# Performance work log

Hardware: AMD Instinct MI355X
Metric: run time of the kernel (lower is better)

The kernel has to match this reference:

```python
import jax, jax.numpy as jnp
import numpy as np

BATCH = 8192
IN_F = 4096
OUT_F = 4096


def setup_inputs() -> dict:
    key = jax.random.key(0)
    k_x, k_w, k_m = jax.random.split(key, 3)
    x = jax.random.normal(k_x, (BATCH, IN_F), dtype=jnp.float32)
    # kaiming_normal_ for relu: std = sqrt(2 / fan_in) with fan_in = in_features
    std = float(np.sqrt(2.0 / IN_F))
    weight = jax.random.normal(k_w, (OUT_F, IN_F), dtype=jnp.float32) * std
    bias = jnp.zeros((OUT_F,), dtype=jnp.float32)
    mask = jax.random.bernoulli(k_m, 0.5, (OUT_F, IN_F)).astype(jnp.float32)
    return {"x": x, "weight": weight, "bias": bias, "mask": mask}


def reference(x, weight, bias, mask):
    # masked_weight = weight * mask; out = x @ masked_weight.T + bias
    masked_weight = weight * mask                      # [out, in]
    return jnp.einsum("bi,oi->bo", x, masked_weight) + bias  # [batch, out]
```

## Files before the change

### kernel.cpp

```cpp
#include <hip/hip_runtime.h>
#include <stdint.h>

#define BATCH 8192
#define IN_F  4096
#define OUT_F 4096

#define BM 256
#define BN 256
#define BK 32
#define KT2 (IN_F / BK)
#define ABYTES (BM * BK * 2)
#define BUFB   (2 * ABYTES)

typedef __attribute__((ext_vector_type(8))) short bf16x8;
typedef __attribute__((ext_vector_type(4))) float f32x4;


__device__ __forceinline__ unsigned short f2bf(float f) {
    unsigned int u = __float_as_uint(f);
    unsigned int lsb = (u >> 16) & 1u;
    u += 0x7fffu + lsb;
    return (unsigned short)(u >> 16);
}

__device__ __forceinline__ void gl_lds16(const void* g, void* l) {
    __builtin_amdgcn_global_load_lds(
        (const __attribute__((address_space(1))) void*)g,
        (__attribute__((address_space(3))) void*)l,
        16, 0, 0);
}

#define XF4 (BATCH * IN_F / 4)
#define WF4 (OUT_F * IN_F / 4)

__global__ __launch_bounds__(256) void cvt_kernel(const float4* __restrict__ x,
                                                  const float4* __restrict__ w,
                                                  const float4* __restrict__ m,
                                                  uint2* __restrict__ xo,
                                                  uint2* __restrict__ wo) {
    const int i = blockIdx.x * 256 + threadIdx.x;
    union { unsigned short u[4]; uint2 v; } r;
    if (i < XF4) {
        const float4 a = x[i];
        r.u[0] = f2bf(a.x); r.u[1] = f2bf(a.y);
        r.u[2] = f2bf(a.z); r.u[3] = f2bf(a.w);
        xo[i] = r.v;
    } else {
        const int j = i - XF4;
        const float4 a = w[j];
        const float4 b = m[j];
        r.u[0] = f2bf(a.x * b.x); r.u[1] = f2bf(a.y * b.y);
        r.u[2] = f2bf(a.z * b.z); r.u[3] = f2bf(a.w * b.w);
        wo[j] = r.v;
    }
}

__global__ __launch_bounds__(512, 2) void gemm_kernel(const unsigned short* __restrict__ A,
                                                      const unsigned short* __restrict__ W,
                                                      const float* __restrict__ bias,
                                                      float* __restrict__ C) {
    __shared__ unsigned short lds[3 * BUFB / 2];

    const int tid  = threadIdx.x;
    const int lane = tid & 63;
    const int wave = tid >> 6;
    const int wm   = wave >> 2;
    const int wn   = wave & 3;

    const int wg = ((blockIdx.x & 7) << 6) | (blockIdx.x >> 3);
    const int bm = wg >> 4;
    const int bn = wg & 15;

    const int r15 = lane & 15;
    const int g   = lane >> 4;
    const int cs  = (g ^ (r15 & 3)) << 4;

    int aoff[8], boff[4];
#pragma unroll
    for (int mf = 0; mf < 8; ++mf)
        aoff[mf] = ((wm * 128 + mf * 16 + r15) << 6) + cs;
#pragma unroll
    for (int nf = 0; nf < 4; ++nf)
        boff[nf] = ABYTES + ((wn * 64 + nf * 16 + r15) << 6) + cs;

    int ldsb[4];
    const unsigned short* gA[2];
    const unsigned short* gB[2];
#pragma unroll
    for (int i = 0; i < 4; ++i) {
        const int s    = (i & 1) * 512 + tid;
        const int row  = s >> 2;
        const int chnk = (s & 3) ^ (row & 3);
        ldsb[i] = (i < 2 ? 0 : ABYTES) + s * 16;
        if (i < 2) gA[i]     = A + (size_t)(bm * BM + row) * IN_F + chnk * 8;
        else       gB[i - 2] = W + (size_t)(bn * BN + row) * IN_F + chnk * 8;
    }

    char* ldsc = (char*)lds;

#define STAGE(bufoff, ktn)                                                   \
    do {                                                                     \
        gl_lds16(gA[0] + (ktn) * BK, ldsc + (bufoff) + ldsb[0]);             \
        gl_lds16(gA[1] + (ktn) * BK, ldsc + (bufoff) + ldsb[1]);             \
        gl_lds16(gB[0] + (ktn) * BK, ldsc + (bufoff) + ldsb[2]);             \
        gl_lds16(gB[1] + (ktn) * BK, ldsc + (bufoff) + ldsb[3]);             \
    } while (0)

#define READ(AX, BX, bufoff)                                                 \
    do {                                                                     \
        _Pragma("unroll")                                                    \
        for (int mf = 0; mf < 8; ++mf)                                       \
            AX[mf] = *(const bf16x8*)(ldsc + (bufoff) + aoff[mf]);           \
        _Pragma("unroll")                                                    \
        for (int nf = 0; nf < 4; ++nf)                                       \
            BX[nf] = *(const bf16x8*)(ldsc + (bufoff) + boff[nf]);           \
    } while (0)

#define MFMA_ALL(AX, BX)                                                     \
    do {                                                                     \
        __builtin_amdgcn_s_setprio(1);                                       \
        _Pragma("unroll")                                                    \
        for (int mf = 0; mf < 8; ++mf)                                       \
            _Pragma("unroll")                                                \
            for (int nf = 0; nf < 4; ++nf)                                   \
                acc[mf][nf] = __builtin_amdgcn_mfma_f32_16x16x32_bf16(       \
                    AX[mf], BX[nf], acc[mf][nf], 0, 0, 0);                   \
        __builtin_amdgcn_s_setprio(0);                                       \
    } while (0)

#define WINDOW(kt, AC, BC, AN, BN_)                                          \
    do {                                                                     \
        if ((kt) + 1 < KT2) READ(AN, BN_, rb);                               \
        if ((kt) + 3 < KT2) STAGE(sb, (kt) + 3);                             \
        MFMA_ALL(AC, BC);                                                    \
        if ((kt) + 1 < KT2) {                                                \
            asm volatile("s_waitcnt lgkmcnt(0)" ::: "memory");               \
            __builtin_amdgcn_sched_barrier(0);                               \
            if ((kt) + 3 < KT2) { asm volatile("s_waitcnt vmcnt(4)" ::: "memory"); } \
            else                { asm volatile("s_waitcnt vmcnt(0)" ::: "memory"); } \
            __builtin_amdgcn_s_barrier();                                    \
            __builtin_amdgcn_sched_barrier(0);                               \
            int t_ = sb; sb = rb; rb = lb; lb = t_;                          \
        }                                                                    \
    } while (0)

    f32x4 acc[8][4] = {};
    bf16x8 aC[8], bC[4], aN[8], bN[4];

    STAGE(0 * BUFB, 0);
    STAGE(1 * BUFB, 1);
    STAGE(2 * BUFB, 2);
    asm volatile("s_waitcnt vmcnt(8)" ::: "memory");
    __builtin_amdgcn_s_barrier();
    __builtin_amdgcn_sched_barrier(0);

    READ(aC, bC, 0 * BUFB);
    asm volatile("s_waitcnt lgkmcnt(0)" ::: "memory");
    __builtin_amdgcn_sched_barrier(0);
    asm volatile("s_waitcnt vmcnt(4)" ::: "memory");
    __builtin_amdgcn_s_barrier();
    __builtin_amdgcn_sched_barrier(0);

    int sb = 0 * BUFB, rb = 1 * BUFB, lb = 2 * BUFB;

#pragma unroll 1
    for (int kt = 0; kt < KT2; kt += 2) {
        WINDOW(kt,     aC, bC, aN, bN);
        WINDOW(kt + 1, aN, bN, aC, bC);
    }
#undef WINDOW
#undef MFMA_ALL
#undef READ
#undef STAGE

    const int crow0 = bm * BM + wm * 128 + g * 4;
    const int ccol0 = bn * BN + wn * 64 + r15;
#pragma unroll
    for (int nf = 0; nf < 4; ++nf) {
        const int col = ccol0 + nf * 16;
        const float bj = bias[col];
#pragma unroll
        for (int mf = 0; mf < 8; ++mf)
#pragma unroll
            for (int reg = 0; reg < 4; ++reg) {
                const int row = crow0 + mf * 16 + reg;
                C[(size_t)row * OUT_F + col] = acc[mf][nf][reg] + bj;
            }
    }
}

__global__ __launch_bounds__(256) void fallback_kernel(const float* __restrict__ x,
                                                       const float* __restrict__ w,
                                                       const float* __restrict__ bias,
                                                       const float* __restrict__ m,
                                                       float* __restrict__ out) {
    size_t idx = (size_t)blockIdx.x * 256 + threadIdx.x;
    int row = (int)(idx >> 12);
    int col = (int)(idx & (OUT_F - 1));
    const float4* xr = (const float4*)(x + (size_t)row * IN_F);
    const float4* wr = (const float4*)(w + (size_t)col * IN_F);
    const float4* mr = (const float4*)(m + (size_t)col * IN_F);
    float s = 0.f;
    for (int k = 0; k < IN_F / 4; ++k) {
        float4 xv = xr[k], wv = wr[k], mv = mr[k];
        s += xv.x * wv.x * mv.x + xv.y * wv.y * mv.y +
             xv.z * wv.z * mv.z + xv.w * wv.w * mv.w;
    }
    out[idx] = s + bias[col];
}


extern "C" void kernel_launch(void* const* d_in, const int* in_sizes, int n_in,
                              void* d_out, int out_size, void* d_ws, size_t ws_size,
                              hipStream_t stream) {
    const float* x    = (const float*)d_in[0];
    const float* w    = (const float*)d_in[1];
    const float* bias = (const float*)d_in[2];
    const float* mask = (const float*)d_in[3];
    float* out = (float*)d_out;

    const size_t need = ((size_t)BATCH * IN_F + (size_t)OUT_F * IN_F) * sizeof(unsigned short);
    if (ws_size < need) {
        fallback_kernel<<<(size_t)BATCH * OUT_F / 256, 256, 0, stream>>>(
            x, w, bias, mask, out);
        return;
    }

    unsigned short* xb = (unsigned short*)d_ws;
    unsigned short* wb = xb + (size_t)BATCH * IN_F;

    cvt_kernel<<<(XF4 + WF4) / 256, 256, 0, stream>>>(
        (const float4*)x, (const float4*)w, (const float4*)mask,
        (uint2*)xb, (uint2*)wb);

    gemm_kernel<<<512, 512, 0, stream>>>(xb, wb, bias, out);
}
```

Before: 557.5 us.

## Switch GEMM to BK=64 double-buffered LDS with four-phase interleaved schedule

Doubles the K tile to 64 and replaces the triple-buffered BK=32 pipeline with two 64KB buffers. Each K step is split into four phases. Each phase reads a slice of A fragments from LDS, issues part of the next tile's global-to-LDS loads, and runs a group of MFMAs, separated by barriers. The goal is fewer loop iterations and barriers per FLOP, a smaller live fragment register set, and a finer mix of memory and MFMA work. The cost is 128KB of LDS per block and more barriers per iteration, which could stall waves if the phases are not balanced.

Result: faster. 541.2 us (-2.9%).

```diff
diff --git a/kernel.cpp b/kernel.cpp
--- a/kernel.cpp
+++ b/kernel.cpp
@@ -7,10 +7,8 @@
 
 #define BM 256
 #define BN 256
-#define BK 32
-#define KT2 (IN_F / BK)
-#define ABYTES (BM * BK * 2)
-#define BUFB   (2 * ABYTES)
+#define BK 64
+#define KT (IN_F / BK)
 
 typedef __attribute__((ext_vector_type(8))) short bf16x8;
 typedef __attribute__((ext_vector_type(4))) float f32x4;
@@ -59,7 +57,9 @@
                                                       const unsigned short* __restrict__ W,
                                                       const float* __restrict__ bias,
                                                       float* __restrict__ C) {
-    __shared__ unsigned short lds[3 * BUFB / 2];
+    __shared__ __align__(16) char smem[131072];
+    char* sA = smem;
+    char* sB = smem + 65536;
 
     const int tid  = threadIdx.x;
     const int lane = tid & 63;
@@ -73,105 +73,115 @@
 
     const int r15 = lane & 15;
     const int g   = lane >> 4;
-    const int cs  = (g ^ (r15 & 3)) << 4;
-
-    int aoff[8], boff[4];
-#pragma unroll
-    for (int mf = 0; mf < 8; ++mf)
-        aoff[mf] = ((wm * 128 + mf * 16 + r15) << 6) + cs;
-#pragma unroll
-    for (int nf = 0; nf < 4; ++nf)
-        boff[nf] = ABYTES + ((wn * 64 + nf * 16 + r15) << 6) + cs;
-
-    int ldsb[4];
-    const unsigned short* gA[2];
-    const unsigned short* gB[2];
+    const int k0  = (g ^ (r15 & 7)) << 4;
+
+    int ldso[4];
+    const unsigned short* gAp[4];
+    const unsigned short* gBp[4];
 #pragma unroll
     for (int i = 0; i < 4; ++i) {
-        const int s    = (i & 1) * 512 + tid;
-        const int row  = s >> 2;
-        const int chnk = (s & 3) ^ (row & 3);
-        ldsb[i] = (i < 2 ? 0 : ABYTES) + s * 16;
-        if (i < 2) gA[i]     = A + (size_t)(bm * BM + row) * IN_F + chnk * 8;
-        else       gB[i - 2] = W + (size_t)(bn * BN + row) * IN_F + chnk * 8;
-    }
-
-    char* ldsc = (char*)lds;
-
-#define STAGE(bufoff, ktn)                                                   \
-    do {                                                                     \
-        gl_lds16(gA[0] + (ktn) * BK, ldsc + (bufoff) + ldsb[0]);             \
-        gl_lds16(gA[1] + (ktn) * BK, ldsc + (bufoff) + ldsb[1]);             \
-        gl_lds16(gB[0] + (ktn) * BK, ldsc + (bufoff) + ldsb[2]);             \
-        gl_lds16(gB[1] + (ktn) * BK, ldsc + (bufoff) + ldsb[3]);             \
-    } while (0)
-
-#define READ(AX, BX, bufoff)                                                 \
+        const int s   = i * 512 + tid;
+        const int row = s >> 3;
+        const int ch  = (s & 7) ^ (row & 7);
+        ldso[i] = s * 16;
+        gAp[i] = A + (size_t)(bm * BM + row) * IN_F + ch * 8;
+        gBp[i] = W + (size_t)(bn * BN + row) * IN_F + ch * 8;
+    }
+
+#define GLA(buf, ktn, sl) gl_lds16(gAp[sl] + (ktn) * BK, sA + (buf) * 32768 + ldso[sl])
+#define GLB(buf, ktn, sl) gl_lds16(gBp[sl] + (ktn) * BK, sB + (buf) * 32768 + ldso[sl])
+
+    f32x4 acc[8][4] = {};
+    bf16x8 af[2][2], bgf[4][2];
+
+#define RDA(p)                                                               \
     do {                                                                     \
         _Pragma("unroll")                                                    \
-        for (int mf = 0; mf < 8; ++mf)                                       \
-            AX[mf] = *(const bf16x8*)(ldsc + (bufoff) + aoff[mf]);           \
+        for (int i = 0; i < 2; ++i)                                          \
+            _Pragma("unroll")                                                \
+            for (int ks = 0; ks < 2; ++ks)                                   \
+                af[i][ks] = *(const bf16x8*)(aB2 + ((p) * 2 + i) * 2048 +    \
+                                             (k0 ^ (ks << 6)));              \
+    } while (0)
+#define RDB()                                                                \
+    do {                                                                     \
         _Pragma("unroll")                                                    \
         for (int nf = 0; nf < 4; ++nf)                                       \
-            BX[nf] = *(const bf16x8*)(ldsc + (bufoff) + boff[nf]);           \
+            _Pragma("unroll")                                                \
+            for (int ks = 0; ks < 2; ++ks)                                   \
+                bgf[nf][ks] = *(const bf16x8*)(bB2 + nf * 2048 +             \
+                                               (k0 ^ (ks << 6)));            \
     } while (0)
-
-#define MFMA_ALL(AX, BX)                                                     \
+#define MM(p)                                                                \
     do {                                                                     \
         __builtin_amdgcn_s_setprio(1);                                       \
         _Pragma("unroll")                                                    \
-        for (int mf = 0; mf < 8; ++mf)                                       \
+        for (int ks = 0; ks < 2; ++ks)                                       \
             _Pragma("unroll")                                                \
-            for (int nf = 0; nf < 4; ++nf)                                   \
-                acc[mf][nf] = __builtin_amdgcn_mfma_f32_16x16x32_bf16(       \
-                    AX[mf], BX[nf], acc[mf][nf], 0, 0, 0);                   \
+            for (int i = 0; i < 2; ++i)                                      \
+                _Pragma("unroll")                                            \
+                for (int nf = 0; nf < 4; ++nf)                               \
+                    acc[(p) * 2 + i][nf] =                                   \
+                        __builtin_amdgcn_mfma_f32_16x16x32_bf16(             \
+                            af[i][ks], bgf[nf][ks], acc[(p) * 2 + i][nf],    \
+                            0, 0, 0);                                        \
         __builtin_amdgcn_s_setprio(0);                                       \
     } while (0)
-
-#define WINDOW(kt, AC, BC, AN, BN_)                                          \
-    do {                                                                     \
-        if ((kt) + 1 < KT2) READ(AN, BN_, rb);                               \
-        if ((kt) + 3 < KT2) STAGE(sb, (kt) + 3);                             \
-        MFMA_ALL(AC, BC);                                                    \
-        if ((kt) + 1 < KT2) {                                                \
-            asm volatile("s_waitcnt lgkmcnt(0)" ::: "memory");               \
-            __builtin_amdgcn_sched_barrier(0);                               \
-            if ((kt) + 3 < KT2) { asm volatile("s_waitcnt vmcnt(4)" ::: "memory"); } \
-            else                { asm volatile("s_waitcnt vmcnt(0)" ::: "memory"); } \
-            __builtin_amdgcn_s_barrier();                                    \
-            __builtin_amdgcn_sched_barrier(0);                               \
-            int t_ = sb; sb = rb; rb = lb; lb = t_;                          \
-        }                                                                    \
-    } while (0)
-
-    f32x4 acc[8][4] = {};
-    bf16x8 aC[8], bC[4], aN[8], bN[4];
-
-    STAGE(0 * BUFB, 0);
-    STAGE(1 * BUFB, 1);
-    STAGE(2 * BUFB, 2);
-    asm volatile("s_waitcnt vmcnt(8)" ::: "memory");
-    __builtin_amdgcn_s_barrier();
-    __builtin_amdgcn_sched_barrier(0);
-
-    READ(aC, bC, 0 * BUFB);
-    asm volatile("s_waitcnt lgkmcnt(0)" ::: "memory");
-    __builtin_amdgcn_sched_barrier(0);
-    asm volatile("s_waitcnt vmcnt(4)" ::: "memory");
-    __builtin_amdgcn_s_barrier();
-    __builtin_amdgcn_sched_barrier(0);
-
-    int sb = 0 * BUFB, rb = 1 * BUFB, lb = 2 * BUFB;
+#define LG0   asm volatile("s_waitcnt lgkmcnt(0)" ::: "memory")
+#define SBAR  __builtin_amdgcn_s_barrier()
+#define SCH0  __builtin_amdgcn_sched_barrier(0)
+
+    GLB(0, 0, 0); GLB(0, 0, 1); GLB(0, 0, 2); GLB(0, 0, 3);
+    GLA(0, 0, 0); GLA(0, 0, 2); GLA(0, 0, 1); GLA(0, 0, 3);
+    asm volatile("s_waitcnt vmcnt(2)" ::: "memory");
+    SBAR; SCH0;
 
 #pragma unroll 1
-    for (int kt = 0; kt < KT2; kt += 2) {
-        WINDOW(kt,     aC, bC, aN, bN);
-        WINDOW(kt + 1, aN, bN, aC, bC);
-    }
-#undef WINDOW
-#undef MFMA_ALL
-#undef READ
-#undef STAGE
+    for (int kt = 0; kt < KT; ++kt) {
+        const int buf  = kt & 1;
+        const int nb   = buf ^ 1;
+        const bool more = (kt + 1 < KT);
+        const char* aB2 = sA + buf * 32768 + ((wm * 128 + r15) << 7);
+        const char* bB2 = sB + buf * 32768 + ((wn * 64 + r15) << 7);
+
+        RDB(); RDA(0);
+        if (more) { GLB(nb, kt + 1, 0); GLB(nb, kt + 1, 1); }
+        asm volatile("s_waitcnt lgkmcnt(8)" ::: "memory");
+        SBAR; LG0; SCH0;
+        MM(0);
+        SCH0; SBAR; SCH0;
+
+        RDA(1);
+        if (more) { GLB(nb, kt + 1, 2); GLB(nb, kt + 1, 3); }
+        SBAR; LG0; SCH0;
+        MM(1);
+        SCH0;
+        if (more) { asm volatile("s_waitcnt vmcnt(4)" ::: "memory"); }
+        else      { asm volatile("s_waitcnt vmcnt(0)" ::: "memory"); }
+        SBAR; SCH0;
+
+        RDA(2);
+        if (more) { GLA(nb, kt + 1, 0); GLA(nb, kt + 1, 2); }
+        SBAR; LG0; SCH0;
+        MM(2);
+        SCH0; SBAR; SCH0;
+
+        RDA(3);
+        if (more) { GLA(nb, kt + 1, 1); GLA(nb, kt + 1, 3); }
+        SBAR; LG0; SCH0;
+        MM(3);
+        SCH0;
+        if (more) { asm volatile("s_waitcnt vmcnt(2)" ::: "memory"); }
+        SBAR; SCH0;
+    }
+#undef GLA
+#undef GLB
+#undef RDA
+#undef RDB
+#undef MM
+#undef LG0
+#undef SBAR
+#undef SCH0
 
     const int crow0 = bm * BM + wm * 128 + g * 4;
     const int ccol0 = bn * BN + wn * 64 + r15;
```
